# Kernel optimization log

Hardware: AMD Instinct MI355X
Metric: run time of the kernel (lower is better)

Reference implementation:

```python
import jax, jax.numpy as jnp
import numpy as np

N_HEADS, D_MODEL, D_HEAD = 16, 1024, 64
EPSILON = -100000.0  # module uses -1e5, not -inf
INIT_STD = 0.02


def setup_inputs() -> dict:
    key = jax.random.key(0)
    ks = jax.random.split(key, 5)
    B, S = 4, 2048
    x = jax.random.normal(ks[0], (B, S, D_MODEL), dtype=jnp.float32)
    W_Q = INIT_STD * jax.random.normal(ks[1], (N_HEADS, D_MODEL, D_HEAD), dtype=jnp.float32)
    W_K = INIT_STD * jax.random.normal(ks[2], (N_HEADS, D_MODEL, D_HEAD), dtype=jnp.float32)
    W_V = INIT_STD * jax.random.normal(ks[3], (N_HEADS, D_MODEL, D_HEAD), dtype=jnp.float32)
    W_O = INIT_STD * jax.random.normal(ks[4], (N_HEADS, D_HEAD, D_MODEL), dtype=jnp.float32)
    b_Q = jnp.zeros((N_HEADS, D_HEAD), jnp.float32)
    b_K = jnp.zeros((N_HEADS, D_HEAD), jnp.float32)
    b_V = jnp.zeros((N_HEADS, D_HEAD), jnp.float32)
    b_O = jnp.zeros((D_MODEL,), jnp.float32)
    return {"normalized_resid_pre": x, "W_Q": W_Q, "b_Q": b_Q, "W_K": W_K,
            "b_K": b_K, "W_V": W_V, "b_V": b_V, "W_O": W_O, "b_O": b_O}


def reference(normalized_resid_pre, W_Q, b_Q, W_K, b_K, W_V, b_V, W_O, b_O):
    x = normalized_resid_pre  # [b, s, e]
    q = jnp.einsum('bse,neh->bsnh', x, W_Q) + b_Q
    k = jnp.einsum('bse,neh->bsnh', x, W_K) + b_K
    v = jnp.einsum('bse,neh->bsnh', x, W_V) + b_V
    scores = jnp.einsum('bqnh,bknh->bnqk', q, k) / jnp.sqrt(jnp.float32(D_HEAD))
    sq, sk = scores.shape[-2], scores.shape[-1]
    causal = jnp.triu(jnp.ones((sq, sk), bool), k=1)  # True above diagonal
    scores = jnp.where(causal, jnp.float32(EPSILON), scores)
    probs = jax.nn.softmax(scores, axis=-1)
    z = jnp.einsum('bnqk,bknh->bqnh', probs, v)
    # sum over heads of per-head output projection + bias
    attn_out = jnp.einsum('bqnh,nhe->bqe', z, W_O) + b_O
    return attn_out
```

## Files before the change

### kernel.cpp

```cpp
#include <hip/hip_runtime.h>


typedef __attribute__((ext_vector_type(8))) short short8;
typedef __attribute__((ext_vector_type(4))) float floatx4;

#define SCL 0.1803368801111244f

__device__ __forceinline__ unsigned short f2bf(float f) {
  unsigned int x = __float_as_uint(f);
  x += 0x7fffu + ((x >> 16) & 1u);
  return (unsigned short)(x >> 16);
}

__device__ __forceinline__ void gload_lds16(const unsigned short* g, unsigned short* lds) {
  __builtin_amdgcn_global_load_lds(
      (const __attribute__((address_space(1))) void*)g,
      (__attribute__((address_space(3))) void*)lds, 16, 0, 0);
}

__global__ __launch_bounds__(256) void prep_kernel(
    const float* __restrict__ X,  unsigned short* __restrict__ Xb,
    const float* __restrict__ Wq, const float* __restrict__ Wk,
    const float* __restrict__ Wv, unsigned short* __restrict__ Bt,
    const float* __restrict__ Wo, unsigned short* __restrict__ Wt)
{
  __shared__ unsigned short T[64 * 72];
  const int bid = blockIdx.x, t = threadIdx.x;
  if (bid < 8192) {
    int idx = ((bid << 8) + t) << 2;
    float4 f = *(const float4*)(X + idx);
    unsigned short u[4] = { f2bf(f.x), f2bf(f.y), f2bf(f.z), f2bf(f.w) };
    *(uint2*)(Xb + idx) = *(uint2*)u;
  } else if (bid < 8960) {
    int b2 = bid - 8192;
    int e0 = (b2 & 15) << 6, nn = (b2 >> 4) & 15, proj = b2 >> 8;
    const float* W = (proj == 0) ? Wq : (proj == 1) ? Wk : Wv;
    const float* src = W + ((size_t)nn << 16) + ((size_t)e0 << 6);
#pragma unroll
    for (int rnd = 0; rnd < 4; ++rnd) {
      int off = (rnd << 10) + (t << 2);
      float4 f = *(const float4*)(src + off);
      int r = off >> 6, h = off & 63;
      T[r * 72 + h]     = f2bf(f.x);
      T[r * 72 + h + 1] = f2bf(f.y);
      T[r * 72 + h + 2] = f2bf(f.z);
      T[r * 72 + h + 3] = f2bf(f.w);
    }
    __syncthreads();
    const int h = t >> 2, ck = t & 3;
    size_t orow = ((size_t)((proj << 10) + (nn << 6) + h) << 10) + e0 + (ck << 4);
#pragma unroll
    for (int g = 0; g < 2; ++g) {
      unsigned short v[8];
#pragma unroll
      for (int j = 0; j < 8; ++j) v[j] = T[((ck << 4) + (g << 3) + j) * 72 + h];
      *(int4*)(Bt + orow + (g << 3)) = *(int4*)v;
    }
  } else {
    int b2 = bid - 8960;
    int e0 = (b2 & 15) << 6, k0 = (b2 >> 4) << 6;
#pragma unroll
    for (int rnd = 0; rnd < 4; ++rnd) {
      int r = (rnd << 4) + (t >> 4);
      int c = (t & 15) << 2;
      float4 f = *(const float4*)(Wo + ((size_t)(k0 + r) << 10) + e0 + c);
      T[r * 72 + c]     = f2bf(f.x);
      T[r * 72 + c + 1] = f2bf(f.y);
      T[r * 72 + c + 2] = f2bf(f.z);
      T[r * 72 + c + 3] = f2bf(f.w);
    }
    __syncthreads();
    const int i = t >> 2, ck = t & 3;
    size_t orow = ((size_t)(e0 + i) << 10) + k0 + (ck << 4);
#pragma unroll
    for (int g = 0; g < 2; ++g) {
      unsigned short v[8];
#pragma unroll
      for (int j = 0; j < 8; ++j) v[j] = T[((ck << 4) + (g << 3) + j) * 72 + i];
      *(int4*)(Wt + orow + (g << 3)) = *(int4*)v;
    }
  }
}

template <int MODE>
__global__ __launch_bounds__(256) void gemm128_kernel(
    const unsigned short* __restrict__ A,
    const unsigned short* __restrict__ Bt,
    const float* __restrict__ b0, const float* __restrict__ b1,
    const float* __restrict__ b2,
    unsigned short* __restrict__ Oq, unsigned short* __restrict__ Ok,
    unsigned short* __restrict__ Ov, float* __restrict__ Of)
{
  const int K = 1024;
  __shared__ __align__(16) unsigned short As[8192];
  __shared__ __align__(16) unsigned short Bs[8192];
  const int tid = threadIdx.x;
  const int l   = tid & 63, w = tid >> 6;
  const int l15 = l & 15,  lg = l >> 4;
  const int mo  = (w >> 1) << 6, no = (w & 1) << 6;
  const int m0  = blockIdx.y << 7, n0 = blockIdx.x << 7;
  const int srow = l >> 3;
  const int gblk = ((l & 7) ^ srow) << 3;
  const int rsw  = l15 & 7;

  floatx4 acc[4][4];
#pragma unroll
  for (int i = 0; i < 4; ++i)
#pragma unroll
    for (int j = 0; j < 4; ++j) acc[i][j] = (floatx4){0.f, 0.f, 0.f, 0.f};

  for (int k0 = 0; k0 < K; k0 += 64) {
    __syncthreads();
#pragma unroll
    for (int s = 0; s < 4; ++s) {
      const int br = (s << 5) + (w << 3);
      gload_lds16(A  + (size_t)(m0 + br + srow) * K + k0 + gblk, &As[br << 6]);
      gload_lds16(Bt + (size_t)(n0 + br + srow) * K + k0 + gblk, &Bs[br << 6]);
    }
    __syncthreads();
#pragma unroll
    for (int kh = 0; kh < 2; ++kh) {
      const int bo = (((kh << 2) + lg) ^ rsw) << 3;
      short8 af[4], bf[4];
#pragma unroll
      for (int mc = 0; mc < 4; ++mc)
        af[mc] = *(const short8*)&As[((mo + (mc << 4) + l15) << 6) + bo];
#pragma unroll
      for (int nc = 0; nc < 4; ++nc)
        bf[nc] = *(const short8*)&Bs[((no + (nc << 4) + l15) << 6) + bo];
#pragma unroll
      for (int mc = 0; mc < 4; ++mc)
#pragma unroll
        for (int nc = 0; nc < 4; ++nc)
          acc[mc][nc] = __builtin_amdgcn_mfma_f32_16x16x32_bf16(af[mc], bf[nc], acc[mc][nc], 0, 0, 0);
    }
  }

#pragma unroll
  for (int nc = 0; nc < 4; ++nc) {
    int c = n0 + no + (nc << 4) + l15;
    if (MODE == 1) {
      float bv = b0[c];
#pragma unroll
      for (int mc = 0; mc < 4; ++mc)
#pragma unroll
        for (int r = 0; r < 4; ++r) {
          int m = m0 + mo + (mc << 4) + (lg << 2) + r;
          Of[((size_t)m << 10) + c] = acc[mc][nc][r] + bv;
        }
    } else {
      int proj = c >> 10, cc = c & 1023;
      int hn = cc >> 6, h = cc & 63;
      const float* bp = (proj == 0) ? b0 : (proj == 1) ? b1 : b2;
      float bv = bp[cc];
      float sc = (proj == 0) ? SCL : 1.0f;
      if (proj < 2) {
        unsigned short* O = (proj == 0) ? Oq : Ok;
#pragma unroll
        for (int mc = 0; mc < 4; ++mc)
#pragma unroll
          for (int r = 0; r < 4; ++r) {
            int m = m0 + mo + (mc << 4) + (lg << 2) + r;
            int bb = m >> 11, ss = m & 2047;
            O[((((size_t)(bb << 4) + hn) << 11) + ss) * 64 + h] = f2bf((acc[mc][nc][r] + bv) * sc);
          }
      } else {
#pragma unroll
        for (int mc = 0; mc < 4; ++mc) {
          int m = m0 + mo + (mc << 4) + (lg << 2);
          int bb = m >> 11, ss = m & 2047;
          unsigned short p0 = f2bf(acc[mc][nc][0] + bv);
          unsigned short p1 = f2bf(acc[mc][nc][1] + bv);
          unsigned short p2 = f2bf(acc[mc][nc][2] + bv);
          unsigned short p3 = f2bf(acc[mc][nc][3] + bv);
          uint2 pk;
          pk.x = (unsigned int)p0 | ((unsigned int)p1 << 16);
          pk.y = (unsigned int)p2 | ((unsigned int)p3 << 16);
          *(uint2*)&Ov[((((size_t)(bb << 4) + hn) << 6) + h) * 2048 + ss] = pk;
        }
      }
    }
  }
}

__global__ __launch_bounds__(128) void flash6_kernel(
    const unsigned short* __restrict__ Q,
    const unsigned short* __restrict__ K,
    const unsigned short* __restrict__ Vt,
    unsigned short* __restrict__ Z)
{
  __shared__ __align__(16) unsigned short Ks[8192];
  __shared__ __align__(16) unsigned short Vs[8192];
  __shared__ __align__(16) unsigned short Ps[4096];

  const int tid = threadIdx.x;
  const int l   = tid & 63, w = tid >> 6;
  const int l15 = l & 15,  lg = l >> 4;
  const int x    = blockIdx.x;
  const int pidx = (x >> 3) & 15;
  const int head = ((x & 7) << 3) + (x >> 7);
  const int n = head & 15, b = head >> 4;
  const size_t hoff = (size_t)head << 17;
  const unsigned short* Qh = Q + hoff;
  const unsigned short* Kh = K + hoff;
  const unsigned short* Vh = Vt + hoff;
  unsigned short* Psw = Ps + (w << 11);

  const int srow8 = l >> 3;
  const int sblk8 = ((l & 7) ^ srow8) << 3;
  const int swz   = l15 & 7;
  const int bo0   = (lg ^ swz) << 3;
  const int bo1   = ((4 + lg) ^ swz) << 3;

  int pwofs[4], profs[2];
#pragma unroll
  for (int mc = 0; mc < 4; ++mc)
    pwofs[mc] = ((((mc << 1) + (lg >> 1)) ^ swz) << 3) + ((lg & 1) << 2);
#pragma unroll
  for (int kc = 0; kc < 2; ++kc)
    profs[kc] = (((kc << 2) + lg) ^ swz) << 3;

  short8 onef;
#pragma unroll
  for (int i = 0; i < 8; ++i) onef[i] = (short)0x3F80;

#pragma unroll
  for (int j = 0; j < 4; ++j) {
    const int s = (w << 2) + j;
    gload_lds16(Kh + (size_t)((s << 3) + srow8) * 64 + sblk8, &Ks[s << 9]);
    gload_lds16(Vh + (size_t)((s << 3) + srow8) * 2048 + sblk8, &Vs[s << 9]);
  }
  asm volatile("s_waitcnt vmcnt(0)" ::: "memory");
  __builtin_amdgcn_s_barrier();

  int buf = 0;
  for (int half = 0; half < 2; ++half) {
    const int qt  = half ? pidx : (31 - pidx);
    const int q0w = (qt << 6) + (w << 5);

    short8 qf[2][2];
#pragma unroll
    for (int qc = 0; qc < 2; ++qc)
#pragma unroll
      for (int dh = 0; dh < 2; ++dh)
        qf[qc][dh] = *(const short8*)(Qh + (size_t)(q0w + (qc << 4) + l15) * 64 + (dh << 5) + (lg << 3));

    floatx4 acc_o[2][4], acc_l[2];
#pragma unroll
    for (int qc = 0; qc < 2; ++qc) {
      acc_l[qc] = (floatx4){0.f, 0.f, 0.f, 0.f};
#pragma unroll
      for (int dc = 0; dc < 4; ++dc) acc_o[qc][dc] = (floatx4){0.f, 0.f, 0.f, 0.f};
    }

    const int nkt = qt + 1;
    for (int kt = 0; kt < nkt; ++kt) {
      int nk0 = (kt + 1 < nkt) ? ((kt + 1) << 6) : (half == 0 ? 0 : -1);
      if (nk0 >= 0) {
        const int nb = (buf ^ 1) << 12;
#pragma unroll
        for (int j = 0; j < 4; ++j) {
          const int s = (w << 2) + j;
          gload_lds16(Kh + (size_t)(nk0 + (s << 3) + srow8) * 64 + sblk8, &Ks[nb + (s << 9)]);
          gload_lds16(Vh + (size_t)((s << 3) + srow8) * 2048 + nk0 + sblk8, &Vs[nb + (s << 9)]);
        }
      }

      const int k0 = kt << 6;
      const int cb = buf << 12;

      floatx4 s0[4], s1[4];
#pragma unroll
      for (int mc = 0; mc < 4; ++mc) {
        s0[mc] = (floatx4){0.f, 0.f, 0.f, 0.f};
        s1[mc] = (floatx4){0.f, 0.f, 0.f, 0.f};
      }
      __builtin_amdgcn_s_setprio(1);
#pragma unroll
      for (int dh = 0; dh < 2; ++dh) {
        const int bo = dh ? bo1 : bo0;
#pragma unroll
        for (int mc = 0; mc < 4; ++mc) {
          short8 ak = *(const short8*)&Ks[cb + (((mc << 4) + l15) << 6) + bo];
          s0[mc] = __builtin_amdgcn_mfma_f32_16x16x32_bf16(ak, qf[0][dh], s0[mc], 0, 0, 0);
          s1[mc] = __builtin_amdgcn_mfma_f32_16x16x32_bf16(ak, qf[1][dh], s1[mc], 0, 0, 0);
        }
      }
      __builtin_amdgcn_s_setprio(0);

      const bool needmask = (k0 + 63 > q0w);
#pragma unroll
      for (int qc = 0; qc < 2; ++qc) {
        const int qg = q0w + (qc << 4) + l15;
        const int rbase = ((qc << 4) + l15) << 6;
#pragma unroll
        for (int mc = 0; mc < 4; ++mc) {
          float p[4];
#pragma unroll
          for (int r = 0; r < 4; ++r) {
            float e = exp2f(qc ? s1[mc][r] : s0[mc][r]);
            if (needmask) {
              int key = k0 + (mc << 4) + (lg << 2) + r;
              e = (key > qg) ? 0.f : e;
            }
            p[r] = e;
          }
          uint2 pk;
          pk.x = (__float_as_uint(p[1]) & 0xFFFF0000u) | (__float_as_uint(p[0]) >> 16);
          pk.y = (__float_as_uint(p[3]) & 0xFFFF0000u) | (__float_as_uint(p[2]) >> 16);
          *(uint2*)&Psw[rbase + pwofs[mc]] = pk;
        }
      }

      short8 pa[2][2];
#pragma unroll
      for (int qc = 0; qc < 2; ++qc) {
        const int rbase = ((qc << 4) + l15) << 6;
#pragma unroll
        for (int kc = 0; kc < 2; ++kc)
          pa[qc][kc] = *(const short8*)&Psw[rbase + profs[kc]];
      }
      __builtin_amdgcn_s_setprio(1);
#pragma unroll
      for (int kc = 0; kc < 2; ++kc) {
        const int bo = kc ? bo1 : bo0;
#pragma unroll
        for (int dc = 0; dc < 4; ++dc) {
          short8 vb = *(const short8*)&Vs[cb + (((dc << 4) + l15) << 6) + bo];
          acc_o[0][dc] = __builtin_amdgcn_mfma_f32_16x16x32_bf16(pa[0][kc], vb, acc_o[0][dc], 0, 0, 0);
          acc_o[1][dc] = __builtin_amdgcn_mfma_f32_16x16x32_bf16(pa[1][kc], vb, acc_o[1][dc], 0, 0, 0);
        }
        acc_l[0] = __builtin_amdgcn_mfma_f32_16x16x32_bf16(pa[0][kc], onef, acc_l[0], 0, 0, 0);
        acc_l[1] = __builtin_amdgcn_mfma_f32_16x16x32_bf16(pa[1][kc], onef, acc_l[1], 0, 0, 0);
      }
      __builtin_amdgcn_s_setprio(0);

      asm volatile("s_waitcnt vmcnt(0)" ::: "memory");
      __builtin_amdgcn_s_barrier();
      buf ^= 1;
    }

#pragma unroll
    for (int qc = 0; qc < 2; ++qc) {
      floatx4 inv;
#pragma unroll
      for (int r = 0; r < 4; ++r) inv[r] = 1.f / acc_l[qc][r];
#pragma unroll
      for (int dc = 0; dc < 4; ++dc)
#pragma unroll
        for (int r = 0; r < 4; ++r) {
          int qg = q0w + (qc << 4) + (lg << 2) + r;
          Z[(((size_t)b << 11) + qg) * 1024 + (n << 6) + (dc << 4) + l15] =
              f2bf(acc_o[qc][dc][r] * inv[r]);
        }
    }
  }
}

extern "C" void kernel_launch(void* const* d_in, const int* in_sizes, int n_in,
                              void* d_out, int out_size, void* d_ws, size_t ws_size,
                              hipStream_t stream) {
  const float* x   = (const float*)d_in[0];
  const float* W_Q = (const float*)d_in[1];
  const float* b_Q = (const float*)d_in[2];
  const float* W_K = (const float*)d_in[3];
  const float* b_K = (const float*)d_in[4];
  const float* W_V = (const float*)d_in[5];
  const float* b_V = (const float*)d_in[6];
  const float* W_O = (const float*)d_in[7];
  const float* b_O = (const float*)d_in[8];
  float* out = (float*)d_out;

  unsigned short* ws    = (unsigned short*)d_ws;
  unsigned short* BtQKV = ws;
  unsigned short* Wo_t  = BtQKV + (3u << 20);
  unsigned short* Xb    = Wo_t + (1u << 20);
  unsigned short* Qb    = Xb + (8u << 20);
  unsigned short* Kb    = Qb + (8u << 20);
  unsigned short* Vtb   = Kb + (8u << 20);
  unsigned short* Zb    = Vtb + (8u << 20);

  prep_kernel<<<9216, 256, 0, stream>>>(x, Xb, W_Q, W_K, W_V, BtQKV, W_O, Wo_t);

  gemm128_kernel<0><<<dim3(24, 64), 256, 0, stream>>>(
      Xb, BtQKV, b_Q, b_K, b_V, Qb, Kb, Vtb, nullptr);

  flash6_kernel<<<1024, 128, 0, stream>>>(Qb, Kb, Vtb, Zb);

  gemm128_kernel<1><<<dim3(8, 64), 256, 0, stream>>>(
      Zb, Wo_t, b_O, nullptr, nullptr, nullptr, nullptr, nullptr, out);
}
```

Before: 276.0 us.

## Load K/V fragments directly from global into registers, drop LDS staging

The flash attention kernel stops staging K and V tiles in shared memory with double-buffered global-to-LDS loads and barriers. Each wave now reads its K and V MFMA operands straight from global memory (relying on L2/L1 for reuse between the two waves). The grid changes from 1024 blocks, each handling a paired long and short query tile, to 2048 blocks with one query tile each, ordered longest-first. Launch bounds request 3 blocks per CU. This removes LDS traffic and barriers and raises occupancy, but duplicates global loads across waves, exposes load latency without explicit prefetch, and loses the causal load-balancing pairing.

```diff
diff --git a/kernel.cpp b/kernel.cpp
--- a/kernel.cpp
+++ b/kernel.cpp
@@ -183,22 +183,20 @@
   }
 }
 
-__global__ __launch_bounds__(128) void flash6_kernel(
+__global__ __launch_bounds__(128, 3) void flash7_kernel(
     const unsigned short* __restrict__ Q,
     const unsigned short* __restrict__ K,
     const unsigned short* __restrict__ Vt,
     unsigned short* __restrict__ Z)
 {
-  __shared__ __align__(16) unsigned short Ks[8192];
-  __shared__ __align__(16) unsigned short Vs[8192];
   __shared__ __align__(16) unsigned short Ps[4096];
 
   const int tid = threadIdx.x;
   const int l   = tid & 63, w = tid >> 6;
   const int l15 = l & 15,  lg = l >> 4;
   const int x    = blockIdx.x;
-  const int pidx = (x >> 3) & 15;
-  const int head = ((x & 7) << 3) + (x >> 7);
+  const int qt   = 31 - (x >> 6);
+  const int head = x & 63;
   const int n = head & 15, b = head >> 4;
   const size_t hoff = (size_t)head << 17;
   const unsigned short* Qh = Q + hoff;
@@ -206,12 +204,7 @@
   const unsigned short* Vh = Vt + hoff;
   unsigned short* Psw = Ps + (w << 11);
 
-  const int srow8 = l >> 3;
-  const int sblk8 = ((l & 7) ^ srow8) << 3;
-  const int swz   = l15 & 7;
-  const int bo0   = (lg ^ swz) << 3;
-  const int bo1   = ((4 + lg) ^ swz) << 3;
-
+  const int swz = l15 & 7;
   int pwofs[4], profs[2];
 #pragma unroll
   for (int mc = 0; mc < 4; ++mc)
@@ -224,136 +217,116 @@
 #pragma unroll
   for (int i = 0; i < 8; ++i) onef[i] = (short)0x3F80;
 
-#pragma unroll
-  for (int j = 0; j < 4; ++j) {
-    const int s = (w << 2) + j;
-    gload_lds16(Kh + (size_t)((s << 3) + srow8) * 64 + sblk8, &Ks[s << 9]);
-    gload_lds16(Vh + (size_t)((s << 3) + srow8) * 2048 + sblk8, &Vs[s << 9]);
-  }
-  asm volatile("s_waitcnt vmcnt(0)" ::: "memory");
-  __builtin_amdgcn_s_barrier();
-
-  int buf = 0;
-  for (int half = 0; half < 2; ++half) {
-    const int qt  = half ? pidx : (31 - pidx);
-    const int q0w = (qt << 6) + (w << 5);
-
-    short8 qf[2][2];
-#pragma unroll
-    for (int qc = 0; qc < 2; ++qc)
-#pragma unroll
-      for (int dh = 0; dh < 2; ++dh)
-        qf[qc][dh] = *(const short8*)(Qh + (size_t)(q0w + (qc << 4) + l15) * 64 + (dh << 5) + (lg << 3));
-
-    floatx4 acc_o[2][4], acc_l[2];
+  const int q0w = (qt << 6) + (w << 5);
+
+  short8 qf[2][2];
+#pragma unroll
+  for (int qc = 0; qc < 2; ++qc)
+#pragma unroll
+    for (int dh = 0; dh < 2; ++dh)
+      qf[qc][dh] = *(const short8*)(Qh + (size_t)(q0w + (qc << 4) + l15) * 64 + (dh << 5) + (lg << 3));
+
+  floatx4 acc_o[2][4], acc_l[2];
+#pragma unroll
+  for (int qc = 0; qc < 2; ++qc) {
+    acc_l[qc] = (floatx4){0.f, 0.f, 0.f, 0.f};
+#pragma unroll
+    for (int dc = 0; dc < 4; ++dc) acc_o[qc][dc] = (floatx4){0.f, 0.f, 0.f, 0.f};
+  }
+
+  const int nkt = qt + 1;
+  for (int kt = 0; kt < nkt; ++kt) {
+    const int k0 = kt << 6;
+
+    short8 ak[2][4];
+#pragma unroll
+    for (int dh = 0; dh < 2; ++dh)
+#pragma unroll
+      for (int mc = 0; mc < 4; ++mc)
+        ak[dh][mc] = *(const short8*)(Kh + (size_t)(k0 + (mc << 4) + l15) * 64 + (dh << 5) + (lg << 3));
+
+    floatx4 s0[4], s1[4];
+#pragma unroll
+    for (int mc = 0; mc < 4; ++mc) {
+      s0[mc] = (floatx4){0.f, 0.f, 0.f, 0.f};
+      s1[mc] = (floatx4){0.f, 0.f, 0.f, 0.f};
+    }
+    __builtin_amdgcn_s_setprio(1);
+#pragma unroll
+    for (int dh = 0; dh < 2; ++dh)
+#pragma unroll
+      for (int mc = 0; mc < 4; ++mc) {
+        s0[mc] = __builtin_amdgcn_mfma_f32_16x16x32_bf16(ak[dh][mc], qf[0][dh], s0[mc], 0, 0, 0);
+        s1[mc] = __builtin_amdgcn_mfma_f32_16x16x32_bf16(ak[dh][mc], qf[1][dh], s1[mc], 0, 0, 0);
+      }
+    __builtin_amdgcn_s_setprio(0);
+
+    short8 vb[2][4];
+#pragma unroll
+    for (int kc = 0; kc < 2; ++kc)
+#pragma unroll
+      for (int dc = 0; dc < 4; ++dc)
+        vb[kc][dc] = *(const short8*)(Vh + (size_t)((dc << 4) + l15) * 2048 + k0 + (kc << 5) + (lg << 3));
+
+    const bool needmask = (k0 + 63 > q0w);
 #pragma unroll
     for (int qc = 0; qc < 2; ++qc) {
-      acc_l[qc] = (floatx4){0.f, 0.f, 0.f, 0.f};
-#pragma unroll
-      for (int dc = 0; dc < 4; ++dc) acc_o[qc][dc] = (floatx4){0.f, 0.f, 0.f, 0.f};
-    }
-
-    const int nkt = qt + 1;
-    for (int kt = 0; kt < nkt; ++kt) {
-      int nk0 = (kt + 1 < nkt) ? ((kt + 1) << 6) : (half == 0 ? 0 : -1);
-      if (nk0 >= 0) {
-        const int nb = (buf ^ 1) << 12;
-#pragma unroll
-        for (int j = 0; j < 4; ++j) {
-          const int s = (w << 2) + j;
-          gload_lds16(Kh + (size_t)(nk0 + (s << 3) + srow8) * 64 + sblk8, &Ks[nb + (s << 9)]);
-          gload_lds16(Vh + (size_t)((s << 3) + srow8) * 2048 + nk0 + sblk8, &Vs[nb + (s << 9)]);
+      const int qg = q0w + (qc << 4) + l15;
+      const int rbase = ((qc << 4) + l15) << 6;
+#pragma unroll
+      for (int mc = 0; mc < 4; ++mc) {
+        float p[4];
+#pragma unroll
+        for (int r = 0; r < 4; ++r) {
+          float e = exp2f(qc ? s1[mc][r] : s0[mc][r]);
+          if (needmask) {
+            int key = k0 + (mc << 4) + (lg << 2) + r;
+            e = (key > qg) ? 0.f : e;
+          }
+          p[r] = e;
         }
-      }
-
-      const int k0 = kt << 6;
-      const int cb = buf << 12;
-
-      floatx4 s0[4], s1[4];
-#pragma unroll
-      for (int mc = 0; mc < 4; ++mc) {
-        s0[mc] = (floatx4){0.f, 0.f, 0.f, 0.f};
-        s1[mc] = (floatx4){0.f, 0.f, 0.f, 0.f};
-      }
-      __builtin_amdgcn_s_setprio(1);
-#pragma unroll
-      for (int dh = 0; dh < 2; ++dh) {
-        const int bo = dh ? bo1 : bo0;
-#pragma unroll
-        for (int mc = 0; mc < 4; ++mc) {
-          short8 ak = *(const short8*)&Ks[cb + (((mc << 4) + l15) << 6) + bo];
-          s0[mc] = __builtin_amdgcn_mfma_f32_16x16x32_bf16(ak, qf[0][dh], s0[mc], 0, 0, 0);
-          s1[mc] = __builtin_amdgcn_mfma_f32_16x16x32_bf16(ak, qf[1][dh], s1[mc], 0, 0, 0);
-        }
-      }
-      __builtin_amdgcn_s_setprio(0);
-
-      const bool needmask = (k0 + 63 > q0w);
-#pragma unroll
-      for (int qc = 0; qc < 2; ++qc) {
-        const int qg = q0w + (qc << 4) + l15;
-        const int rbase = ((qc << 4) + l15) << 6;
-#pragma unroll
-        for (int mc = 0; mc < 4; ++mc) {
-          float p[4];
-#pragma unroll
-          for (int r = 0; r < 4; ++r) {
-            float e = exp2f(qc ? s1[mc][r] : s0[mc][r]);
-            if (needmask) {
-              int key = k0 + (mc << 4) + (lg << 2) + r;
-              e = (key > qg) ? 0.f : e;
-            }
-            p[r] = e;
-          }
-          uint2 pk;
-          pk.x = (__float_as_uint(p[1]) & 0xFFFF0000u) | (__float_as_uint(p[0]) >> 16);
-          pk.y = (__float_as_uint(p[3]) & 0xFFFF0000u) | (__float_as_uint(p[2]) >> 16);
-          *(uint2*)&Psw[rbase + pwofs[mc]] = pk;
-        }
-      }
-
-      short8 pa[2][2];
-#pragma unroll
-      for (int qc = 0; qc < 2; ++qc) {
-        const int rbase = ((qc << 4) + l15) << 6;
-#pragma unroll
-        for (int kc = 0; kc < 2; ++kc)
-          pa[qc][kc] = *(const short8*)&Psw[rbase + profs[kc]];
-      }
-      __builtin_amdgcn_s_setprio(1);
-#pragma unroll
-      for (int kc = 0; kc < 2; ++kc) {
-        const int bo = kc ? bo1 : bo0;
-#pragma unroll
-        for (int dc = 0; dc < 4; ++dc) {
-          short8 vb = *(const short8*)&Vs[cb + (((dc << 4) + l15) << 6) + bo];
-          acc_o[0][dc] = __builtin_amdgcn_mfma_f32_16x16x32_bf16(pa[0][kc], vb, acc_o[0][dc], 0, 0, 0);
-          acc_o[1][dc] = __builtin_amdgcn_mfma_f32_16x16x32_bf16(pa[1][kc], vb, acc_o[1][dc], 0, 0, 0);
-        }
-        acc_l[0] = __builtin_amdgcn_mfma_f32_16x16x32_bf16(pa[0][kc], onef, acc_l[0], 0, 0, 0);
-        acc_l[1] = __builtin_amdgcn_mfma_f32_16x16x32_bf16(pa[1][kc], onef, acc_l[1], 0, 0, 0);
-      }
-      __builtin_amdgcn_s_setprio(0);
-
-      asm volatile("s_waitcnt vmcnt(0)" ::: "memory");
-      __builtin_amdgcn_s_barrier();
-      buf ^= 1;
-    }
-
+        uint2 pk;
+        pk.x = (__float_as_uint(p[1]) & 0xFFFF0000u) | (__float_as_uint(p[0]) >> 16);
+        pk.y = (__float_as_uint(p[3]) & 0xFFFF0000u) | (__float_as_uint(p[2]) >> 16);
+        *(uint2*)&Psw[rbase + pwofs[mc]] = pk;
+      }
+    }
+
+    short8 pa[2][2];
 #pragma unroll
     for (int qc = 0; qc < 2; ++qc) {
-      floatx4 inv;
-#pragma unroll
-      for (int r = 0; r < 4; ++r) inv[r] = 1.f / acc_l[qc][r];
-#pragma unroll
-      for (int dc = 0; dc < 4; ++dc)
-#pragma unroll
-        for (int r = 0; r < 4; ++r) {
-          int qg = q0w + (qc << 4) + (lg << 2) + r;
-          Z[(((size_t)b << 11) + qg) * 1024 + (n << 6) + (dc << 4) + l15] =
-              f2bf(acc_o[qc][dc][r] * inv[r]);
-        }
-    }
+      const int rbase = ((qc << 4) + l15) << 6;
+#pragma unroll
+      for (int kc = 0; kc < 2; ++kc)
+        pa[qc][kc] = *(const short8*)&Psw[rbase + profs[kc]];
+    }
+    __builtin_amdgcn_s_setprio(1);
+#pragma unroll
+    for (int kc = 0; kc < 2; ++kc) {
+#pragma unroll
+      for (int dc = 0; dc < 4; ++dc) {
+        acc_o[0][dc] = __builtin_amdgcn_mfma_f32_16x16x32_bf16(pa[0][kc], vb[kc][dc], acc_o[0][dc], 0, 0, 0);
+        acc_o[1][dc] = __builtin_amdgcn_mfma_f32_16x16x32_bf16(pa[1][kc], vb[kc][dc], acc_o[1][dc], 0, 0, 0);
+      }
+      acc_l[0] = __builtin_amdgcn_mfma_f32_16x16x32_bf16(pa[0][kc], onef, acc_l[0], 0, 0, 0);
+      acc_l[1] = __builtin_amdgcn_mfma_f32_16x16x32_bf16(pa[1][kc], onef, acc_l[1], 0, 0, 0);
+    }
+    __builtin_amdgcn_s_setprio(0);
+  }
+
+#pragma unroll
+  for (int qc = 0; qc < 2; ++qc) {
+    floatx4 inv;
+#pragma unroll
+    for (int r = 0; r < 4; ++r) inv[r] = 1.f / acc_l[qc][r];
+#pragma unroll
+    for (int dc = 0; dc < 4; ++dc)
+#pragma unroll
+      for (int r = 0; r < 4; ++r) {
+        int qg = q0w + (qc << 4) + (lg << 2) + r;
+        Z[(((size_t)b << 11) + qg) * 1024 + (n << 6) + (dc << 4) + l15] =
+            f2bf(acc_o[qc][dc][r] * inv[r]);
+      }
   }
 }
 
@@ -385,7 +358,7 @@
   gemm128_kernel<0><<<dim3(24, 64), 256, 0, stream>>>(
       Xb, BtQKV, b_Q, b_K, b_V, Qb, Kb, Vtb, nullptr);
 
-  flash6_kernel<<<1024, 128, 0, stream>>>(Qb, Kb, Vtb, Zb);
+  flash7_kernel<<<2048, 128, 0, stream>>>(Qb, Kb, Vtb, Zb);
 
   gemm128_kernel<1><<<dim3(8, 64), 256, 0, stream>>>(
       Zb, Wo_t, b_O, nullptr, nullptr, nullptr, nullptr, nullptr, out);
```

Result: slower. 332.1 us (+20.3%).
